# Kernel optimization log

Hardware: AMD Instinct MI355X
Metric: run time of the kernel (lower is better)

Reference implementation:

```python
import jax, jax.numpy as jnp
import numpy as np

PATCH = 16
CH = 3


def setup_inputs() -> dict:
    key = jax.random.key(0)
    k1, k2, k3 = jax.random.split(key, 3)
    B, H = 16, 512
    embed_dim = PATCH * PATCH * CH  # 768
    x = jax.random.normal(k1, (B, CH, H, H), dtype=jnp.float32)
    fan_in = CH * PATCH * PATCH
    w = jax.random.normal(k2, (embed_dim, CH, PATCH, PATCH), dtype=jnp.float32) / np.float32(np.sqrt(fan_in))
    b = jax.random.normal(k3, (embed_dim,), dtype=jnp.float32) * 0.01
    return {"x": x, "w": w, "b": b}


def reference(x, w, b):
    p = w.shape[2]                      # patch_size
    B, C, imgsize, _ = x.shape
    pn = imgsize // p                   # patch_num (NOTE: pre-padding count, as in source)
    # zero-pad by one patch on every side
    xp = jnp.pad(x, ((0, 0), (0, 0), (p, p), (p, p)))
    # strided patch-embed conv: [B, embed_dim, pn+2, pn+2]
    xt = jax.lax.conv_general_dilated(xp, w, window_strides=(p, p), padding='VALID')
    xt = xt + b[None, :, None, None]
    B1, C1, H1, W1 = xt.shape           # H1 = W1 = pn + 2
    xt = xt.reshape(B1, C1, H1 * W1)
    # same (buggy-looking but faithful) index set / stride-pn neighbors as the source
    idxs = jnp.array([i * pn + j for i in range(1, pn - 1) for j in range(1, pn)], dtype=jnp.int32)
    inv8 = jnp.float32(1.0 / 8.0)

    def body(buf, idx):
        # torch aliases x_final=x_temp, so reads see earlier in-place writes -> sequential scan
        s = (buf[:, :, idx - pn] + buf[:, :, idx + pn]
             + buf[:, :, idx - 1] + buf[:, :, idx + 1]
             + buf[:, :, idx - pn - 1] + buf[:, :, idx - pn + 1]
             + buf[:, :, idx + pn - 1] + buf[:, :, idx + pn + 1]) * inv8
        return buf.at[:, :, idx].set(s), None

    xf, _ = jax.lax.scan(body, xt, idxs)
    side = imgsize + 2 * p              # embed_dim*H1*W1 == C*side*side by construction
    out = xf.reshape(B1, C, side, side)
    return out[:, :, p:imgsize + p, p:imgsize + p]
```

## Files before the change

kernel.cpp:

```cpp
#include <hip/hip_runtime.h>
#include <hip/hip_bf16.h>


typedef __attribute__((ext_vector_type(8))) short s8v;
typedef __attribute__((ext_vector_type(4))) float f4v;
typedef __attribute__((ext_vector_type(8))) unsigned short us8;
typedef __attribute__((ext_vector_type(4))) unsigned short us4;

__device__ __forceinline__ unsigned short f2bf(float f) {
    __hip_bfloat16 h = __float2bfloat16(f);
    return *reinterpret_cast<unsigned short*>(&h);
}
__device__ __forceinline__ float bf2f(unsigned short u) {
    union { unsigned int i; float f; } c; c.i = (unsigned int)u << 16; return c.f;
}

__global__ __launch_bounds__(256) void prep_w_k(const float* __restrict__ w,
                                                unsigned short* __restrict__ w_bf) {
    int g = blockIdx.x * 256 + threadIdx.x;
    int f = g << 3;
    const float4 v0 = *(const float4*)(w + f);
    const float4 v1 = *(const float4*)(w + f + 4);
    us8 u;
    u[0] = f2bf(v0.x); u[1] = f2bf(v0.y); u[2] = f2bf(v0.z); u[3] = f2bf(v0.w);
    u[4] = f2bf(v1.x); u[5] = f2bf(v1.y); u[6] = f2bf(v1.z); u[7] = f2bf(v1.w);
    *(us8*)(w_bf + f) = u;
}

__global__ __launch_bounds__(512, 4) void conv_gemm_rs_k(const float* __restrict__ x,
                                                         const unsigned short* __restrict__ W,
                                                         const float* __restrict__ bias,
                                                         unsigned short* __restrict__ xt) {
    __shared__ __align__(16) unsigned short As[2][128 * 32];
    __shared__ __align__(16) unsigned short Bs[2][192 * 32];
    const int tid  = threadIdx.x;
    const int lane = tid & 63, wv = tid >> 6;
    const int wr = wv >> 2, wc = wv & 3;
    const int m0 = blockIdx.x << 7;
    const int n0 = blockIdx.y * 192;
    const int bb = m0 >> 10;
    const int ph0 = (m0 >> 5) & 31;

    const int arow = tid >> 2, ach = tid & 3;
    const int phl  = arow >> 5, pw = arow & 31;
    const int aoff = (arow << 5) + ((ach ^ ((arow >> 1) & 3)) << 3);
    const float* xbase = x + (size_t)bb * 786432 + (ph0 + phl) * 8192
                           + (ach >> 1) * 512 + (pw << 4) + ((ach & 1) << 3);

    const int brow = tid >> 1, bpair = tid & 1;
    const int bxr  = (brow >> 1) & 3;
    const int boff0 = (brow << 5) + ((((bpair << 1))     ^ bxr) << 3);
    const int boff1 = (brow << 5) + ((((bpair << 1) | 1) ^ bxr) << 3);
    const unsigned short* wbase = W + (size_t)(n0 + brow) * 768 + (bpair << 4);

    float4 xr_[2][2];
    us8    wf_[2][2];

    auto gload = [&](int s, int t) {
        const float* sp = xbase + (t >> 3) * 262144 + (t & 7) * 1024;
        xr_[s][0] = *(const float4*)(sp);
        xr_[s][1] = *(const float4*)(sp + 4);
        if (tid < 384) {
            const unsigned short* ws = wbase + (t << 5);
            wf_[s][0] = *(const us8*)(ws);
            wf_[s][1] = *(const us8*)(ws + 8);
        }
    };
    auto store = [&](int s, int buf) {
        us8 lo;
        lo[0]=f2bf(xr_[s][0].x); lo[1]=f2bf(xr_[s][0].y);
        lo[2]=f2bf(xr_[s][0].z); lo[3]=f2bf(xr_[s][0].w);
        lo[4]=f2bf(xr_[s][1].x); lo[5]=f2bf(xr_[s][1].y);
        lo[6]=f2bf(xr_[s][1].z); lo[7]=f2bf(xr_[s][1].w);
        *(us8*)(As[buf] + aoff) = lo;
        if (tid < 384) {
            *(us8*)(Bs[buf] + boff0) = wf_[s][0];
            *(us8*)(Bs[buf] + boff1) = wf_[s][1];
        }
    };

    f4v acc[4][3] = {};
    gload(0, 0);
    store(0, 0);
    __syncthreads();

    const int cq = lane >> 4, l15 = lane & 15;
    #pragma unroll
    for (int t = 0; t < 24; ++t) {
        const int p = t & 1;
        if (t < 23) gload(p ^ 1, t + 1);
        s8v a[4], b[3];
        #pragma unroll
        for (int mi = 0; mi < 4; ++mi) {
            int ra = (wr << 6) + (mi << 4) + l15;
            a[mi] = *(const s8v*)(As[p] + (ra << 5) + ((cq ^ ((ra >> 1) & 3)) << 3));
        }
        #pragma unroll
        for (int ni = 0; ni < 3; ++ni) {
            int rb = wc * 48 + (ni << 4) + l15;
            b[ni] = *(const s8v*)(Bs[p] + (rb << 5) + ((cq ^ ((rb >> 1) & 3)) << 3));
        }
        #pragma unroll
        for (int mi = 0; mi < 4; ++mi)
            #pragma unroll
            for (int ni = 0; ni < 3; ++ni)
                acc[mi][ni] = __builtin_amdgcn_mfma_f32_16x16x32_bf16(a[mi], b[ni], acc[mi][ni], 0, 0, 0);
        if (t < 23) store(p ^ 1, p ^ 1);
        __syncthreads();
    }

    #pragma unroll
    for (int mi = 0; mi < 4; ++mi) {
        int m  = m0 + (wr << 6) + (mi << 4) + (cq << 2);
        int ph = (m >> 5) & 31, pwm = m & 31;
        unsigned short* dst = xt + (((size_t)bb * 768) << 10) + (ph << 5) + pwm;
        #pragma unroll
        for (int ni = 0; ni < 3; ++ni) {
            int n = n0 + wc * 48 + (ni << 4) + l15;
            float bv = bias[n];
            us4 o;
            o[0] = f2bf(acc[mi][ni][0] + bv);
            o[1] = f2bf(acc[mi][ni][1] + bv);
            o[2] = f2bf(acc[mi][ni][2] + bv);
            o[3] = f2bf(acc[mi][ni][3] + bv);
            *(us4*)(dst + ((size_t)n << 10)) = o;
        }
    }
}

__global__ __launch_bounds__(256) void scan_emit_k(const unsigned short* __restrict__ xt,
                                                   const float* __restrict__ bias,
                                                   float* __restrict__ out) {
    const int grp = (blockIdx.x * 256 + threadIdx.x) >> 5;
    const int j   = threadIdx.x & 31;
    const int b   = grp / 768;
    const int c1  = grp - b * 768;
    const unsigned short* basep = xt + ((size_t)grp << 10);
    const float bias_c = bias[c1];
    float* baseo = out + (size_t)b * 786432 + (size_t)(c1 >> 8) * 262144;

    int rem = (c1 & 255) * 1156 + j;
    int ey  = rem / 544;
    int ex  = rem - ey * 544;
    int eo  = (ey - 16) * 512 + (ex - 16);

    auto estep = [&](float v) {
        if (((unsigned)(ex - 16) < 512u) & ((unsigned)(ey - 16) < 512u))
            baseo[eo] = v;
        ex += 32;
        int wrp = (ex >= 544);
        ex -= wrp ? 544 : 0;
        ey += wrp;
        eo += wrp ? 0 : 32;
    };
    auto sel = [&](int p) -> float {
        unsigned int h = (unsigned int)p / 34u;
        unsigned int w = (unsigned int)p - h * 34u;
        if ((h == 0u) | (h == 33u) | (w == 0u) | (w == 33u)) return bias_c;
        return bf2f(basep[(h - 1u) * 32u + (w - 1u)]);
    };

    float co = sel( 32 + j);
    float no = sel( 64 + j);
    float o2 = sel( 96 + j);
    float o3 = sel(128 + j);
    estep(bias_c);
    float pn   = bias_c;
    float po_h = bias_c;
    float h_co = __shfl(co, 0, 32);
    float h_no = __shfl(no, 0, 32);
    float h_o2 = __shfl(o2, 0, 32);
    float rr   = __shfl_down(co, 1, 32);
    if (j == 31) rr = h_no;

    int pr  = 160 + j;
    int ph_ = pr / 34;
    int pw_ = pr - ph_ * 34;

    for (int i = 1; i <= 30; ++i) {
        bool bord = (pw_ == 0) | (pw_ == 33);
        float ld = bord ? bias_c : bf2f(basep[(ph_ - 1) * 32 + (pw_ - 1)]);
        pw_ += 32;
        if (pw_ >= 34) { pw_ -= 34; ++ph_; }

        float UL = __shfl_up(pn, 1, 32);   if (j == 1)  UL = po_h;
        float UR = __shfl_down(pn, 1, 32); if (j == 31) UR = h_co;
        float D1 = __shfl_up(no, 1, 32);
        float D3 = __shfl_down(no, 1, 32); if (j == 31) D3 = h_o2;
        float bv = (((UL + pn) + (UR + rr)) + ((D1 + no) + D3)) * 0.125f;
        if (j == 1) bv += h_co * 0.125f;
        float t;
        t = __shfl_up(bv, 1, 32);  bv += (j > 1) ? 0.125f * t : 0.f;
        t = __shfl_up(bv, 2, 32);  bv += (j > 2) ? 0.015625f * t : 0.f;
        t = __shfl_up(bv, 4, 32);  bv += (j > 4) ? 2.44140625e-4f * t : 0.f;
        estep((j == 0) ? co : bv);
        rr   = D3;
        pn   = bv;
        po_h = h_co; h_co = h_no; h_no = h_o2;
        h_o2 = __shfl(o3, 0, 32);
        co = no; no = o2; o2 = o3; o3 = ld;
    }
    estep(co);
    estep(no);
    estep(o2);
    estep(o3);
    estep(sel(1120 + j));
    if (j < 4) estep(bias_c);
}

extern "C" void kernel_launch(void* const* d_in, const int* in_sizes, int n_in,
                              void* d_out, int out_size, void* d_ws, size_t ws_size,
                              hipStream_t stream) {
    const float* x    = (const float*)d_in[0];
    const float* w    = (const float*)d_in[1];
    const float* bias = (const float*)d_in[2];
    float* out = (float*)d_out;
    unsigned short* xt = (unsigned short*)d_ws;

    unsigned short* w_bf = (unsigned short*)d_out;

    prep_w_k<<<288, 256, 0, stream>>>(w, w_bf);
    conv_gemm_rs_k<<<dim3(128, 4), 512, 0, stream>>>(x, w_bf, bias, xt);
    scan_emit_k<<<1536, 256, 0, stream>>>(xt, bias, out);
}
```

Baseline: 68.37 us.

## Split conv GEMM K dimension across two blocks and sum partials in scan

Adds a split-K dimension to the patch-embed GEMM grid. Two blocks each handle half of the 24 K-steps and write separate bf16 partial outputs to two halves of the workspace, with the bias added only by the first half. The scan kernel loads and sums both partials. This doubles the GEMM block count (512 to 1024) to fill more CUs, at the cost of twice the intermediate writes and reads. Rounding each partial to bf16 also adds some precision loss.

```diff
diff --git a/kernel.cpp b/kernel.cpp
--- a/kernel.cpp
+++ b/kernel.cpp
@@ -6,6 +6,8 @@
 typedef __attribute__((ext_vector_type(4))) float f4v;
 typedef __attribute__((ext_vector_type(8))) unsigned short us8;
 typedef __attribute__((ext_vector_type(4))) unsigned short us4;
+
+#define XT_HALF ((size_t)12288 * 1024)
 
 __device__ __forceinline__ unsigned short f2bf(float f) {
     __hip_bfloat16 h = __float2bfloat16(f);
@@ -38,6 +40,8 @@
     const int wr = wv >> 2, wc = wv & 3;
     const int m0 = blockIdx.x << 7;
     const int n0 = blockIdx.y * 192;
+    const int kz = blockIdx.z;
+    const int kbase = kz * 12;
     const int bb = m0 >> 10;
     const int ph0 = (m0 >> 5) & 31;
 
@@ -80,15 +84,15 @@
     };
 
     f4v acc[4][3] = {};
-    gload(0, 0);
+    gload(0, kbase);
     store(0, 0);
     __syncthreads();
 
     const int cq = lane >> 4, l15 = lane & 15;
     #pragma unroll
-    for (int t = 0; t < 24; ++t) {
-        const int p = t & 1;
-        if (t < 23) gload(p ^ 1, t + 1);
+    for (int tt = 0; tt < 12; ++tt) {
+        const int p = tt & 1;
+        if (tt < 11) gload(p ^ 1, kbase + tt + 1);
         s8v a[4], b[3];
         #pragma unroll
         for (int mi = 0; mi < 4; ++mi) {
@@ -105,19 +109,21 @@
             #pragma unroll
             for (int ni = 0; ni < 3; ++ni)
                 acc[mi][ni] = __builtin_amdgcn_mfma_f32_16x16x32_bf16(a[mi], b[ni], acc[mi][ni], 0, 0, 0);
-        if (t < 23) store(p ^ 1, p ^ 1);
+        if (tt < 11) store(p ^ 1, p ^ 1);
         __syncthreads();
     }
 
+    unsigned short* xth = xt + (size_t)kz * XT_HALF;
+    const float bsc = kz ? 0.f : 1.f;
     #pragma unroll
     for (int mi = 0; mi < 4; ++mi) {
         int m  = m0 + (wr << 6) + (mi << 4) + (cq << 2);
         int ph = (m >> 5) & 31, pwm = m & 31;
-        unsigned short* dst = xt + (((size_t)bb * 768) << 10) + (ph << 5) + pwm;
+        unsigned short* dst = xth + (((size_t)bb * 768) << 10) + (ph << 5) + pwm;
         #pragma unroll
         for (int ni = 0; ni < 3; ++ni) {
             int n = n0 + wc * 48 + (ni << 4) + l15;
-            float bv = bias[n];
+            float bv = bsc * bias[n];
             us4 o;
             o[0] = f2bf(acc[mi][ni][0] + bv);
             o[1] = f2bf(acc[mi][ni][1] + bv);
@@ -135,7 +141,8 @@
     const int j   = threadIdx.x & 31;
     const int b   = grp / 768;
     const int c1  = grp - b * 768;
-    const unsigned short* basep = xt + ((size_t)grp << 10);
+    const unsigned short* b0 = xt + ((size_t)grp << 10);
+    const unsigned short* b1 = b0 + XT_HALF;
     const float bias_c = bias[c1];
     float* baseo = out + (size_t)b * 786432 + (size_t)(c1 >> 8) * 262144;
 
@@ -153,11 +160,14 @@
         ey += wrp;
         eo += wrp ? 0 : 32;
     };
+    auto val = [&](int idx) -> float {
+        return bf2f(b0[idx]) + bf2f(b1[idx]);
+    };
     auto sel = [&](int p) -> float {
         unsigned int h = (unsigned int)p / 34u;
         unsigned int w = (unsigned int)p - h * 34u;
         if ((h == 0u) | (h == 33u) | (w == 0u) | (w == 33u)) return bias_c;
-        return bf2f(basep[(h - 1u) * 32u + (w - 1u)]);
+        return val((h - 1u) * 32u + (w - 1u));
     };
 
     float co = sel( 32 + j);
@@ -179,7 +189,7 @@
 
     for (int i = 1; i <= 30; ++i) {
         bool bord = (pw_ == 0) | (pw_ == 33);
-        float ld = bord ? bias_c : bf2f(basep[(ph_ - 1) * 32 + (pw_ - 1)]);
+        float ld = bord ? bias_c : val((ph_ - 1) * 32 + (pw_ - 1));
         pw_ += 32;
         if (pw_ >= 34) { pw_ -= 34; ++ph_; }
 
@@ -220,6 +230,6 @@
     unsigned short* w_bf = (unsigned short*)d_out;
 
     prep_w_k<<<288, 256, 0, stream>>>(w, w_bf);
-    conv_gemm_rs_k<<<dim3(128, 4), 512, 0, stream>>>(x, w_bf, bias, xt);
+    conv_gemm_rs_k<<<dim3(128, 4, 2), 512, 0, stream>>>(x, w_bf, bias, xt);
     scan_emit_k<<<1536, 256, 0, stream>>>(xt, bias, out);
 }
```

Measured after the change: 76.99 us. 12.6% more time.

## Give each wave private LDS tiles and drop block-wide barriers in conv GEMM

Applied to the files above, without the earlier changes.

The conv GEMM kernel now has each wave load and convert only the A (64 rows) and B (48 rows) slices it consumes into its own LDS region. Because no wave reads another wave's data, the per-step __syncthreads and the shared double buffer are removed. The cost is redundant work: waves sharing a row or column of the tile each fetch and convert the same data, so A traffic and fp32-to-bf16 conversion rise about fourfold and B fetches about twofold. LDS use per block also grows, which may lower occupancy.

```diff
diff --git a/kernel.cpp b/kernel.cpp
--- a/kernel.cpp
+++ b/kernel.cpp
@@ -27,12 +27,12 @@
     *(us8*)(w_bf + f) = u;
 }
 
-__global__ __launch_bounds__(512, 4) void conv_gemm_rs_k(const float* __restrict__ x,
+__global__ __launch_bounds__(512, 4) void conv_gemm_wp_k(const float* __restrict__ x,
                                                          const unsigned short* __restrict__ W,
                                                          const float* __restrict__ bias,
                                                          unsigned short* __restrict__ xt) {
-    __shared__ __align__(16) unsigned short As[2][128 * 32];
-    __shared__ __align__(16) unsigned short Bs[2][192 * 32];
+    __shared__ __align__(16) unsigned short Aw[8][64 * 32];
+    __shared__ __align__(16) unsigned short Bw[8][48 * 32];
     const int tid  = threadIdx.x;
     const int lane = tid & 63, wv = tid >> 6;
     const int wr = wv >> 2, wc = wv & 3;
@@ -41,72 +41,82 @@
     const int bb = m0 >> 10;
     const int ph0 = (m0 >> 5) & 31;
 
-    const int arow = tid >> 2, ach = tid & 3;
-    const int phl  = arow >> 5, pw = arow & 31;
-    const int aoff = (arow << 5) + ((ach ^ ((arow >> 1) & 3)) << 3);
-    const float* xbase = x + (size_t)bb * 786432 + (ph0 + phl) * 8192
-                           + (ach >> 1) * 512 + (pw << 4) + ((ach & 1) << 3);
-
-    const int brow = tid >> 1, bpair = tid & 1;
-    const int bxr  = (brow >> 1) & 3;
-    const int boff0 = (brow << 5) + ((((bpair << 1))     ^ bxr) << 3);
-    const int boff1 = (brow << 5) + ((((bpair << 1) | 1) ^ bxr) << 3);
-    const unsigned short* wbase = W + (size_t)(n0 + brow) * 768 + (bpair << 4);
-
-    float4 xr_[2][2];
-    us8    wf_[2][2];
-
-    auto gload = [&](int s, int t) {
-        const float* sp = xbase + (t >> 3) * 262144 + (t & 7) * 1024;
-        xr_[s][0] = *(const float4*)(sp);
-        xr_[s][1] = *(const float4*)(sp + 4);
-        if (tid < 384) {
-            const unsigned short* ws = wbase + (t << 5);
-            wf_[s][0] = *(const us8*)(ws);
-            wf_[s][1] = *(const us8*)(ws + 8);
-        }
-    };
-    auto store = [&](int s, int buf) {
-        us8 lo;
-        lo[0]=f2bf(xr_[s][0].x); lo[1]=f2bf(xr_[s][0].y);
-        lo[2]=f2bf(xr_[s][0].z); lo[3]=f2bf(xr_[s][0].w);
-        lo[4]=f2bf(xr_[s][1].x); lo[5]=f2bf(xr_[s][1].y);
-        lo[6]=f2bf(xr_[s][1].z); lo[7]=f2bf(xr_[s][1].w);
-        *(us8*)(As[buf] + aoff) = lo;
-        if (tid < 384) {
-            *(us8*)(Bs[buf] + boff0) = wf_[s][0];
-            *(us8*)(Bs[buf] + boff1) = wf_[s][1];
-        }
+    unsigned short* aw = Aw[wv];
+    unsigned short* bw = Bw[wv];
+
+    const int chk  = lane & 3;
+    const int rsub = lane >> 2;
+    const int sA   = chk ^ ((lane >> 3) & 3);
+    const int offq = (rsub << 5) + (sA << 3);
+
+    const float* asrc[4];
+    #pragma unroll
+    for (int q = 0; q < 4; ++q) {
+        int row = (q << 4) + rsub;
+        asrc[q] = x + (size_t)bb * 786432
+                    + (ph0 + (wr << 1) + (row >> 5)) * 8192
+                    + ((row & 31) << 4) + ((chk & 1) << 3);
+    }
+    const unsigned short* bsrc[3];
+    #pragma unroll
+    for (int q = 0; q < 3; ++q)
+        bsrc[q] = W + (size_t)(n0 + wc * 48 + (q << 4) + rsub) * 768 + (chk << 3);
+
+    float4 ar[4][2];
+    us8    br[3];
+
+    auto gload = [&](int t) {
+        #pragma unroll
+        for (int q = 0; q < 4; ++q) {
+            int ka = (t << 2) + chk;
+            const float* sp = asrc[q] + ((ka >> 5) << 18) + (((ka >> 1) & 15) << 9);
+            ar[q][0] = *(const float4*)(sp);
+            ar[q][1] = *(const float4*)(sp + 4);
+        }
+        #pragma unroll
+        for (int q = 0; q < 3; ++q)
+            br[q] = *(const us8*)(bsrc[q] + (t << 5));
+    };
+    auto store = [&]() {
+        #pragma unroll
+        for (int q = 0; q < 4; ++q) {
+            us8 o;
+            o[0]=f2bf(ar[q][0].x); o[1]=f2bf(ar[q][0].y);
+            o[2]=f2bf(ar[q][0].z); o[3]=f2bf(ar[q][0].w);
+            o[4]=f2bf(ar[q][1].x); o[5]=f2bf(ar[q][1].y);
+            o[6]=f2bf(ar[q][1].z); o[7]=f2bf(ar[q][1].w);
+            *(us8*)(aw + (q << 9) + offq) = o;
+        }
+        #pragma unroll
+        for (int q = 0; q < 3; ++q)
+            *(us8*)(bw + (q << 9) + offq) = br[q];
     };
 
     f4v acc[4][3] = {};
-    gload(0, 0);
-    store(0, 0);
-    __syncthreads();
+    gload(0);
+    store();
 
     const int cq = lane >> 4, l15 = lane & 15;
     #pragma unroll
     for (int t = 0; t < 24; ++t) {
-        const int p = t & 1;
-        if (t < 23) gload(p ^ 1, t + 1);
+        if (t < 23) gload(t + 1);
         s8v a[4], b[3];
         #pragma unroll
         for (int mi = 0; mi < 4; ++mi) {
-            int ra = (wr << 6) + (mi << 4) + l15;
-            a[mi] = *(const s8v*)(As[p] + (ra << 5) + ((cq ^ ((ra >> 1) & 3)) << 3));
+            int ra = (mi << 4) + l15;
+            a[mi] = *(const s8v*)(aw + (ra << 5) + ((cq ^ ((ra >> 1) & 3)) << 3));
         }
         #pragma unroll
         for (int ni = 0; ni < 3; ++ni) {
-            int rb = wc * 48 + (ni << 4) + l15;
-            b[ni] = *(const s8v*)(Bs[p] + (rb << 5) + ((cq ^ ((rb >> 1) & 3)) << 3));
+            int rb = (ni << 4) + l15;
+            b[ni] = *(const s8v*)(bw + (rb << 5) + ((cq ^ ((rb >> 1) & 3)) << 3));
         }
         #pragma unroll
         for (int mi = 0; mi < 4; ++mi)
             #pragma unroll
             for (int ni = 0; ni < 3; ++ni)
                 acc[mi][ni] = __builtin_amdgcn_mfma_f32_16x16x32_bf16(a[mi], b[ni], acc[mi][ni], 0, 0, 0);
-        if (t < 23) store(p ^ 1, p ^ 1);
-        __syncthreads();
+        if (t < 23) store();
     }
 
     #pragma unroll
@@ -220,6 +230,6 @@
     unsigned short* w_bf = (unsigned short*)d_out;
 
     prep_w_k<<<288, 256, 0, stream>>>(w, w_bf);
-    conv_gemm_rs_k<<<dim3(128, 4), 512, 0, stream>>>(x, w_bf, bias, xt);
+    conv_gemm_wp_k<<<dim3(128, 4), 512, 0, stream>>>(x, w_bf, bias, xt);
     scan_emit_k<<<1536, 256, 0, stream>>>(xt, bias, out);
 }
```

Measured after the change: 107.6 us. 1.57x slower.
